# Kernel optimization log

Measured on AMD Instinct MI355X. Metric: run time of the kernel, lower is better.

Reference implementation:

```python
import jax, jax.numpy as jnp
import numpy as np

N_NODES = 100000
N_EDGES = 1000000
D_IN = 64
D_MODEL = 64  # H * D
H = 4
D = D_MODEL // H


def setup_inputs() -> dict:
    key = jax.random.key(0)
    ks = jax.random.split(key, 9)
    nodes = jax.random.normal(ks[0], (N_NODES, D_IN), dtype=jnp.float32)
    senders = jax.random.randint(ks[1], (N_EDGES,), 0, N_NODES, dtype=jnp.int32)
    receivers = jnp.sort(jax.random.randint(ks[2], (N_EDGES,), 0, N_NODES, dtype=jnp.int32))
    s = 1.0 / np.sqrt(D_IN)
    W_qk = jax.random.uniform(ks[3], (D_IN, D_MODEL), jnp.float32, -s, s)
    b_qk = jnp.zeros((D_MODEL,), jnp.float32)
    W_v = jax.random.uniform(ks[4], (D_IN, D_MODEL), jnp.float32, -s, s)
    b_v = jnp.zeros((D_MODEL,), jnp.float32)
    so = 1.0 / np.sqrt(D_MODEL)
    W_out = jax.random.uniform(ks[5], (D_MODEL, D_MODEL), jnp.float32, -so, so)
    b_out = jnp.zeros((D_MODEL,), jnp.float32)
    return {
        'nodes': nodes, 'W_qk': W_qk, 'b_qk': b_qk, 'W_v': W_v, 'b_v': b_v,
        'W_out': W_out, 'b_out': b_out, 'senders': senders, 'receivers': receivers,
    }


def _segment_softmax(logits, segment_ids, num_segments):
    # jraph-style numerically stable segment softmax (segments are sorted)
    maxs = jax.ops.segment_max(logits, segment_ids, num_segments, indices_are_sorted=True)
    e = jnp.exp(logits - maxs[segment_ids])
    z = jax.ops.segment_sum(e, segment_ids, num_segments, indices_are_sorted=True)
    return e / z[segment_ids]


def reference(nodes, W_qk, b_qk, W_v, b_v, W_out, b_out, senders, receivers):
    N = nodes.shape[0]
    # projections: N (H D) -> N H D
    qks = (nodes @ W_qk + b_qk).reshape(N, H, D)
    vs = (nodes @ W_v + b_v).reshape(N, H, D)
    # per-edge QK scores: [E, H]
    scores = jnp.einsum('ehd,ehd->eh', qks[receivers], qks[senders])
    attn = _segment_softmax(scores, receivers, N)
    # weighted message scatter: [E,H,D] -> [N, H*D]
    messages = (attn[..., None] * vs[senders]).reshape(-1, H * D)
    ctx = jax.ops.segment_sum(messages, receivers, N, indices_are_sorted=True)
    out = ctx @ W_out + b_out
    return out, attn
```

## Files before the change

### kernel.cpp

```cpp
#include <hip/hip_runtime.h>
#include <math.h>


typedef _Float16 h2 __attribute__((ext_vector_type(2)));
typedef _Float16 half8 __attribute__((ext_vector_type(8)));
typedef float floatx4 __attribute__((ext_vector_type(4)));

#define SP_ROW 136

__global__ __launch_bounds__(256) void mhga_prep(
    const float* __restrict__ Wqk, const float* __restrict__ Wv,
    const float* __restrict__ Wout, _Float16* __restrict__ Wt,
    const int* __restrict__ receivers, int* __restrict__ row_ptr,
    int N, int E)
{
    if ((int)blockIdx.x < 48) {
        const int idx = blockIdx.x * 256 + threadIdx.x;
        const int n = idx >> 6, k = idx & 63;
        const float w = (n < 64) ? Wqk[k * 64 + n]
                      : (n < 128) ? Wv[k * 64 + (n - 64)]
                      : Wout[k * 64 + (n - 128)];
        Wt[idx] = (_Float16)w;
        return;
    }
    const int n = (blockIdx.x - 48) * 256 + threadIdx.x;
    if (n > N) return;
    int lo = 0, hi = E;
    while (lo < hi) {
        const int mid = (lo + hi) >> 1;
        if (receivers[mid] < n) lo = mid + 1; else hi = mid;
    }
    row_ptr[n] = lo;
}

__global__ __launch_bounds__(256) void mhga_proj(
    const float* __restrict__ X, const _Float16* __restrict__ Wt,
    const float* __restrict__ bqk, const float* __restrict__ bv,
    unsigned char* __restrict__ packed, int N)
{
    __shared__ __align__(16) _Float16 sP[64 * SP_ROW];
    const int t = threadIdx.x;
    const int w = t >> 6, lane = t & 63;
    const int ln = lane & 15, quad = lane >> 4;
    const int m0 = blockIdx.x * 64;

    const int arow = min(m0 + w * 16 + ln, N - 1);
    const float* xr = X + (size_t)arow * 64;
    const float4 xa = *(const float4*)(xr + quad * 8);
    const float4 xb = *(const float4*)(xr + quad * 8 + 4);
    const float4 xc = *(const float4*)(xr + 32 + quad * 8);
    const float4 xd = *(const float4*)(xr + 32 + quad * 8 + 4);
    const half8 a0 = { (_Float16)xa.x, (_Float16)xa.y, (_Float16)xa.z,
                       (_Float16)xa.w, (_Float16)xb.x, (_Float16)xb.y,
                       (_Float16)xb.z, (_Float16)xb.w };
    const half8 a1 = { (_Float16)xc.x, (_Float16)xc.y, (_Float16)xc.z,
                       (_Float16)xc.w, (_Float16)xd.x, (_Float16)xd.y,
                       (_Float16)xd.z, (_Float16)xd.w };

    floatx4 acc[8];
#pragma unroll
    for (int tt = 0; tt < 8; ++tt) {
        const _Float16* wrow = Wt + (tt * 16 + ln) * 64;
        const half8 b0 = *(const half8*)(wrow + quad * 8);
        const half8 b1 = *(const half8*)(wrow + 32 + quad * 8);
        floatx4 c = {0.f, 0.f, 0.f, 0.f};
        c = __builtin_amdgcn_mfma_f32_16x16x32_f16(a0, b0, c, 0, 0, 0);
        c = __builtin_amdgcn_mfma_f32_16x16x32_f16(a1, b1, c, 0, 0, 0);
        acc[tt] = c;
    }

#pragma unroll
    for (int tt = 0; tt < 8; ++tt) {
        const float bt = (tt < 4) ? bqk[tt * 16 + ln] : bv[(tt - 4) * 16 + ln];
        const int j = (tt & 3) * 16 + ln;
        const int fidx = (j >> 2) * 8 + ((tt < 4) ? 0 : 4) + (j & 3);
#pragma unroll
        for (int r = 0; r < 4; ++r) {
            const int lrow = w * 16 + quad * 4 + r;
            sP[lrow * SP_ROW + fidx] = (_Float16)(acc[tt][r] + bt);
        }
    }

    const int crow = w * 16 + (lane >> 2);
    const int grow = m0 + crow;
    if (grow < N) {
        const _Float16* src = sP + crow * SP_ROW + (lane & 3) * 32;
        unsigned char* dst = packed + (size_t)grow * 256 + (lane & 3) * 64;
#pragma unroll
        for (int c = 0; c < 4; ++c)
            *(uint4*)(dst + c * 16) = *(const uint4*)(src + c * 8);
    }
}

__global__ __launch_bounds__(256) void mhga_attn(
    const unsigned char* __restrict__ packed,
    const int* __restrict__ senders, const int* __restrict__ row_ptr,
    _Float16* __restrict__ ctxb, float* __restrict__ attn_out, int N)
{
    __shared__ float sAtt[4][256];
    const int t = threadIdx.x;
    const int wave = t >> 6, lane = t & 63;
    const int g = lane >> 4, tl = lane & 15;

    for (int n = blockIdx.x * 4 + wave; n < N; n += gridDim.x * 4) {
        const int e0 = row_ptr[n];
        const int e1 = row_ptr[n + 1];
        const int cnt = e1 - e0;

        float l = 0.f;
        float4 ctx = make_float4(0.f, 0.f, 0.f, 0.f);
        const uint4 qpk = *(const uint4*)(packed + (size_t)n * 256 + tl * 16);
        const h2 q0 = __builtin_bit_cast(h2, qpk.x);
        const h2 q1 = __builtin_bit_cast(h2, qpk.y);

        if (cnt <= 64) {
            int sid = 0;
            if (e0 + lane < e1) sid = senders[e0 + lane];
            const int iters = (cnt + 3) >> 2;
            const int s0 = __shfl(sid, g, 64);
            uint4 pk = *(const uint4*)(packed + (size_t)s0 * 256 + tl * 16);
            for (int i = 0; i < iters; ++i) {
                uint4 pkn = pk;
                if (i + 1 < iters) {
                    const int sn = __shfl(sid, (i + 1) * 4 + g, 64);
                    pkn = *(const uint4*)(packed + (size_t)sn * 256 + tl * 16);
                }
                const int idx = i * 4 + g;
                const h2 k0 = __builtin_bit_cast(h2, pk.x);
                const h2 k1 = __builtin_bit_cast(h2, pk.y);
                const h2 v0 = __builtin_bit_cast(h2, pk.z);
                const h2 v1 = __builtin_bit_cast(h2, pk.w);
                float d = __builtin_amdgcn_fdot2(q0, k0, 0.f, false);
                d = __builtin_amdgcn_fdot2(q1, k1, d, false);
                d += __shfl_xor(d, 1, 64);
                d += __shfl_xor(d, 2, 64);
                float p = __expf(d);
                p = (idx < cnt) ? p : 0.f;
                if ((tl & 3) == 0)
                    sAtt[wave][idx * 4 + (tl >> 2)] = p;
                l += p;
                ctx.x = fmaf(p, (float)v0.x, ctx.x);
                ctx.y = fmaf(p, (float)v0.y, ctx.y);
                ctx.z = fmaf(p, (float)v1.x, ctx.z);
                ctx.w = fmaf(p, (float)v1.y, ctx.w);
                pk = pkn;
            }
        } else {
            for (int base = e0; base < e1; base += 64) {
                const int c2 = min(64, e1 - base);
                int sid2 = 0;
                if (base + lane < e1) sid2 = senders[base + lane];
                const int it2 = (c2 + 3) >> 2;
                for (int i = 0; i < it2; ++i) {
                    const int idx = i * 4 + g;
                    const int s = __shfl(sid2, idx, 64);
                    if (idx < c2) {
                        const uint4 pk =
                            *(const uint4*)(packed + (size_t)s * 256 + tl * 16);
                        const h2 k0 = __builtin_bit_cast(h2, pk.x);
                        const h2 k1 = __builtin_bit_cast(h2, pk.y);
                        const h2 v0 = __builtin_bit_cast(h2, pk.z);
                        const h2 v1 = __builtin_bit_cast(h2, pk.w);
                        float d = __builtin_amdgcn_fdot2(q0, k0, 0.f, false);
                        d = __builtin_amdgcn_fdot2(q1, k1, d, false);
                        d += __shfl_xor(d, 1, 64);
                        d += __shfl_xor(d, 2, 64);
                        const float p = __expf(d);
                        if ((tl & 3) == 0)
                            attn_out[(size_t)(base + idx) * 4 + (tl >> 2)] = p;
                        l += p;
                        ctx.x = fmaf(p, (float)v0.x, ctx.x);
                        ctx.y = fmaf(p, (float)v0.y, ctx.y);
                        ctx.z = fmaf(p, (float)v1.x, ctx.z);
                        ctx.w = fmaf(p, (float)v1.y, ctx.w);
                    }
                }
            }
        }

#pragma unroll
        for (int mask = 16; mask <= 32; mask <<= 1) {
            l     += __shfl_xor(l, mask, 64);
            ctx.x += __shfl_xor(ctx.x, mask, 64);
            ctx.y += __shfl_xor(ctx.y, mask, 64);
            ctx.z += __shfl_xor(ctx.z, mask, 64);
            ctx.w += __shfl_xor(ctx.w, mask, 64);
        }
        const float inv = (l > 0.f) ? (1.f / l) : 0.f;

        const float lh = __shfl(l, (lane & 3) << 2, 64);
        const float invl = (lh > 0.f) ? (1.f / lh) : 0.f;
        if (cnt <= 64) {
            const int cnt4 = cnt * 4;
            for (int f = lane; f < cnt4; f += 64)
                attn_out[e0 * 4 + f] = sAtt[wave][f] * invl;
        } else {
            __builtin_amdgcn_s_waitcnt(0x0F70);
            volatile const float* vp = attn_out;
            for (int f = e0 * 4 + lane; f < e1 * 4; f += 64)
                attn_out[f] = vp[f] * invl;
        }

        if (g == 0) {
            const h2 c01 = { (_Float16)(ctx.x * inv), (_Float16)(ctx.y * inv) };
            const h2 c23 = { (_Float16)(ctx.z * inv), (_Float16)(ctx.w * inv) };
            uint2 pc;
            pc.x = __builtin_bit_cast(unsigned int, c01);
            pc.y = __builtin_bit_cast(unsigned int, c23);
            *(uint2*)(ctxb + (size_t)n * 64 + tl * 4) = pc;
        }
    }
}

__global__ __launch_bounds__(256) void mhga_out(
    const _Float16* __restrict__ ctxb, const _Float16* __restrict__ Wt,
    const float* __restrict__ bout, float* __restrict__ out, int N)
{
    const int t = threadIdx.x;
    const int w = t >> 6, lane = t & 63;
    const int ln = lane & 15, quad = lane >> 4;
    const int m0 = blockIdx.x * 64;

    const int arow = min(m0 + w * 16 + ln, N - 1);
    const _Float16* ar = ctxb + (size_t)arow * 64;
    const half8 a0 = *(const half8*)(ar + quad * 8);
    const half8 a1 = *(const half8*)(ar + 32 + quad * 8);

    floatx4 acc[4];
#pragma unroll
    for (int tt = 0; tt < 4; ++tt) {
        const _Float16* wrow = Wt + (size_t)(128 + tt * 16 + ln) * 64;
        const half8 b0 = *(const half8*)(wrow + quad * 8);
        const half8 b1 = *(const half8*)(wrow + 32 + quad * 8);
        floatx4 c = {0.f, 0.f, 0.f, 0.f};
        c = __builtin_amdgcn_mfma_f32_16x16x32_f16(a0, b0, c, 0, 0, 0);
        c = __builtin_amdgcn_mfma_f32_16x16x32_f16(a1, b1, c, 0, 0, 0);
        acc[tt] = c;
    }

#pragma unroll
    for (int tt = 0; tt < 4; ++tt) {
        const float bt = bout[tt * 16 + ln];
#pragma unroll
        for (int r = 0; r < 4; ++r) {
            const int grow = m0 + w * 16 + quad * 4 + r;
            if (grow < N)
                out[(size_t)grow * 64 + tt * 16 + ln] = acc[tt][r] + bt;
        }
    }
}

extern "C" void kernel_launch(void* const* d_in, const int* in_sizes, int n_in,
                              void* d_out, int out_size, void* d_ws, size_t ws_size,
                              hipStream_t stream) {
    const float* nodes   = (const float*)d_in[0];
    const float* W_qk    = (const float*)d_in[1];
    const float* b_qk    = (const float*)d_in[2];
    const float* W_v     = (const float*)d_in[3];
    const float* b_v     = (const float*)d_in[4];
    const float* W_out   = (const float*)d_in[5];
    const float* b_out   = (const float*)d_in[6];
    const int* senders   = (const int*)d_in[7];
    const int* receivers = (const int*)d_in[8];

    const int N = in_sizes[0] / 64;
    const int E = in_sizes[7];

    float* out      = (float*)d_out;
    float* attn_out = out + (size_t)N * 64;

    unsigned char* packed = (unsigned char*)d_ws;
    int*   rowp = (int*)(packed + (size_t)N * 256);
    float* spare = (float*)(rowp + (((N + 1) + 3) & ~3));
    _Float16* ctxb = (_Float16*)spare;
    _Float16* Wt = (_Float16*)(spare + (size_t)E * 4);

    const int RB = (N + 1 + 255) / 256;
    mhga_prep<<<48 + RB, 256, 0, stream>>>(W_qk, W_v, W_out, Wt,
                                           receivers, rowp, N, E);
    mhga_proj<<<(N + 63) / 64, 256, 0, stream>>>(nodes, Wt, b_qk, b_v,
                                                 packed, N);
    mhga_attn<<<2048, 256, 0, stream>>>(packed, senders, rowp,
                                        ctxb, attn_out, N);
    mhga_out<<<(N + 63) / 64, 256, 0, stream>>>(ctxb, Wt, b_out, out, N);
}
```

Measured before the change: 195.5 us.

## Fuse output projection into attention kernel and move row_ptr search into proj

The attention kernel now gives each wave 16 consecutive nodes. It keeps their fp16 context rows in shared memory and runs the output-projection MFMA directly, so the separate mhga_out kernel and the global ctxb round trip go away. The row_ptr binary search moves from the prep kernel into extra blocks of the projection kernel, which shrinks prep to the weight transpose. Fixed per-wave node ranges replace the grid-stride loop, so load balance across waves may be worse when node degrees vary.

```diff
diff --git a/kernel.cpp b/kernel.cpp
--- a/kernel.cpp
+++ b/kernel.cpp
@@ -10,34 +10,35 @@
 
 __global__ __launch_bounds__(256) void mhga_prep(
     const float* __restrict__ Wqk, const float* __restrict__ Wv,
-    const float* __restrict__ Wout, _Float16* __restrict__ Wt,
-    const int* __restrict__ receivers, int* __restrict__ row_ptr,
-    int N, int E)
+    const float* __restrict__ Wout, _Float16* __restrict__ Wt)
 {
-    if ((int)blockIdx.x < 48) {
-        const int idx = blockIdx.x * 256 + threadIdx.x;
-        const int n = idx >> 6, k = idx & 63;
-        const float w = (n < 64) ? Wqk[k * 64 + n]
-                      : (n < 128) ? Wv[k * 64 + (n - 64)]
-                      : Wout[k * 64 + (n - 128)];
-        Wt[idx] = (_Float16)w;
-        return;
-    }
-    const int n = (blockIdx.x - 48) * 256 + threadIdx.x;
-    if (n > N) return;
-    int lo = 0, hi = E;
-    while (lo < hi) {
-        const int mid = (lo + hi) >> 1;
-        if (receivers[mid] < n) lo = mid + 1; else hi = mid;
-    }
-    row_ptr[n] = lo;
+    const int idx = blockIdx.x * 256 + threadIdx.x;
+    const int n = idx >> 6, k = idx & 63;
+    const float w = (n < 64) ? Wqk[k * 64 + n]
+                  : (n < 128) ? Wv[k * 64 + (n - 64)]
+                  : Wout[k * 64 + (n - 128)];
+    Wt[idx] = (_Float16)w;
 }
 
 __global__ __launch_bounds__(256) void mhga_proj(
     const float* __restrict__ X, const _Float16* __restrict__ Wt,
     const float* __restrict__ bqk, const float* __restrict__ bv,
-    unsigned char* __restrict__ packed, int N)
+    unsigned char* __restrict__ packed,
+    const int* __restrict__ receivers, int* __restrict__ row_ptr,
+    int N, int E, int PB)
 {
+    if ((int)blockIdx.x >= PB) {
+        const int n = (blockIdx.x - PB) * 256 + threadIdx.x;
+        if (n > N) return;
+        int lo = 0, hi = E;
+        while (lo < hi) {
+            const int mid = (lo + hi) >> 1;
+            if (receivers[mid] < n) lo = mid + 1; else hi = mid;
+        }
+        row_ptr[n] = lo;
+        return;
+    }
+
     __shared__ __align__(16) _Float16 sP[64 * SP_ROW];
     const int t = threadIdx.x;
     const int w = t >> 6, lane = t & 63;
@@ -95,14 +96,19 @@
 __global__ __launch_bounds__(256) void mhga_attn(
     const unsigned char* __restrict__ packed,
     const int* __restrict__ senders, const int* __restrict__ row_ptr,
-    _Float16* __restrict__ ctxb, float* __restrict__ attn_out, int N)
+    const _Float16* __restrict__ Wt, const float* __restrict__ bout,
+    float* __restrict__ out, float* __restrict__ attn_out, int N)
 {
     __shared__ float sAtt[4][256];
+    __shared__ __align__(16) _Float16 sC[4][16][72];
     const int t = threadIdx.x;
     const int wave = t >> 6, lane = t & 63;
     const int g = lane >> 4, tl = lane & 15;
-
-    for (int n = blockIdx.x * 4 + wave; n < N; n += gridDim.x * 4) {
+    const int base_n = blockIdx.x * 64 + wave * 16;
+
+    for (int i = 0; i < 16; ++i) {
+        const int n = base_n + i;
+        if (n >= N) break;
         const int e0 = row_ptr[n];
         const int e1 = row_ptr[n + 1];
         const int cnt = e1 - e0;
@@ -119,13 +125,13 @@
             const int iters = (cnt + 3) >> 2;
             const int s0 = __shfl(sid, g, 64);
             uint4 pk = *(const uint4*)(packed + (size_t)s0 * 256 + tl * 16);
-            for (int i = 0; i < iters; ++i) {
+            for (int it = 0; it < iters; ++it) {
                 uint4 pkn = pk;
-                if (i + 1 < iters) {
-                    const int sn = __shfl(sid, (i + 1) * 4 + g, 64);
+                if (it + 1 < iters) {
+                    const int sn = __shfl(sid, (it + 1) * 4 + g, 64);
                     pkn = *(const uint4*)(packed + (size_t)sn * 256 + tl * 16);
                 }
-                const int idx = i * 4 + g;
+                const int idx = it * 4 + g;
                 const h2 k0 = __builtin_bit_cast(h2, pk.x);
                 const h2 k1 = __builtin_bit_cast(h2, pk.y);
                 const h2 v0 = __builtin_bit_cast(h2, pk.z);
@@ -151,8 +157,8 @@
                 int sid2 = 0;
                 if (base + lane < e1) sid2 = senders[base + lane];
                 const int it2 = (c2 + 3) >> 2;
-                for (int i = 0; i < it2; ++i) {
-                    const int idx = i * 4 + g;
+                for (int ii = 0; ii < it2; ++ii) {
+                    const int idx = ii * 4 + g;
                     const int s = __shfl(sid2, idx, 64);
                     if (idx < c2) {
                         const uint4 pk =
@@ -207,45 +213,26 @@
             uint2 pc;
             pc.x = __builtin_bit_cast(unsigned int, c01);
             pc.y = __builtin_bit_cast(unsigned int, c23);
-            *(uint2*)(ctxb + (size_t)n * 64 + tl * 4) = pc;
-        }
-    }
-}
-
-__global__ __launch_bounds__(256) void mhga_out(
-    const _Float16* __restrict__ ctxb, const _Float16* __restrict__ Wt,
-    const float* __restrict__ bout, float* __restrict__ out, int N)
-{
-    const int t = threadIdx.x;
-    const int w = t >> 6, lane = t & 63;
-    const int ln = lane & 15, quad = lane >> 4;
-    const int m0 = blockIdx.x * 64;
-
-    const int arow = min(m0 + w * 16 + ln, N - 1);
-    const _Float16* ar = ctxb + (size_t)arow * 64;
-    const half8 a0 = *(const half8*)(ar + quad * 8);
-    const half8 a1 = *(const half8*)(ar + 32 + quad * 8);
-
-    floatx4 acc[4];
+            *(uint2*)(&sC[wave][i][tl * 4]) = pc;
+        }
+    }
+
+    const half8 a0 = *(const half8*)(&sC[wave][tl][g * 8]);
+    const half8 a1 = *(const half8*)(&sC[wave][tl][32 + g * 8]);
 #pragma unroll
     for (int tt = 0; tt < 4; ++tt) {
-        const _Float16* wrow = Wt + (size_t)(128 + tt * 16 + ln) * 64;
-        const half8 b0 = *(const half8*)(wrow + quad * 8);
-        const half8 b1 = *(const half8*)(wrow + 32 + quad * 8);
+        const _Float16* wrow = Wt + (size_t)(128 + tt * 16 + tl) * 64;
+        const half8 b0 = *(const half8*)(wrow + g * 8);
+        const half8 b1 = *(const half8*)(wrow + 32 + g * 8);
         floatx4 c = {0.f, 0.f, 0.f, 0.f};
         c = __builtin_amdgcn_mfma_f32_16x16x32_f16(a0, b0, c, 0, 0, 0);
         c = __builtin_amdgcn_mfma_f32_16x16x32_f16(a1, b1, c, 0, 0, 0);
-        acc[tt] = c;
-    }
-
-#pragma unroll
-    for (int tt = 0; tt < 4; ++tt) {
-        const float bt = bout[tt * 16 + ln];
+        const float bt = bout[tt * 16 + tl];
 #pragma unroll
         for (int r = 0; r < 4; ++r) {
-            const int grow = m0 + w * 16 + quad * 4 + r;
+            const int grow = base_n + g * 4 + r;
             if (grow < N)
-                out[(size_t)grow * 64 + tt * 16 + ln] = acc[tt][r] + bt;
+                out[(size_t)grow * 64 + tt * 16 + tl] = c[r] + bt;
         }
     }
 }
@@ -272,15 +259,13 @@
     unsigned char* packed = (unsigned char*)d_ws;
     int*   rowp = (int*)(packed + (size_t)N * 256);
     float* spare = (float*)(rowp + (((N + 1) + 3) & ~3));
-    _Float16* ctxb = (_Float16*)spare;
     _Float16* Wt = (_Float16*)(spare + (size_t)E * 4);
 
+    const int PB = (N + 63) / 64;
     const int RB = (N + 1 + 255) / 256;
-    mhga_prep<<<48 + RB, 256, 0, stream>>>(W_qk, W_v, W_out, Wt,
-                                           receivers, rowp, N, E);
-    mhga_proj<<<(N + 63) / 64, 256, 0, stream>>>(nodes, Wt, b_qk, b_v,
-                                                 packed, N);
-    mhga_attn<<<2048, 256, 0, stream>>>(packed, senders, rowp,
-                                        ctxb, attn_out, N);
-    mhga_out<<<(N + 63) / 64, 256, 0, stream>>>(ctxb, Wt, b_out, out, N);
-}
+    mhga_prep<<<48, 256, 0, stream>>>(W_qk, W_v, W_out, Wt);
+    mhga_proj<<<PB + RB, 256, 0, stream>>>(nodes, Wt, b_qk, b_v, packed,
+                                           receivers, rowp, N, E, PB);
+    mhga_attn<<<PB, 256, 0, stream>>>(packed, senders, rowp, Wt, b_out,
+                                      out, attn_out, N);
+}
```

Result: no change. 199.4 us (+2.0%).
